# Kernel optimization log

Hardware: AMD Instinct MI355X
Metric: run time of the kernel (lower is better)

Reference implementation:

```python
import jax, jax.numpy as jnp
import numpy as np
import math

NUM_SECTORS = 8
HIDDEN = 128
FEAT = 64
MAX_DIST = 10.0


def gru_last(x, Wih, Whh, bih, bhh):
    # PyTorch GRU (gate order r,z,n); x: (B,T,D) -> last hidden (B,H)
    B = x.shape[0]
    H = Whh.shape[1]
    xp = jnp.einsum('btd,gd->btg', x, Wih) + bih  # (B,T,3H)

    def step(h, xpt):
        hp = h @ Whh.T + bhh
        xr, xz, xn = jnp.split(xpt, 3, -1)
        hr, hz, hn = jnp.split(hp, 3, -1)
        r = jax.nn.sigmoid(xr + hr)
        z = jax.nn.sigmoid(xz + hz)
        n = jnp.tanh(xn + r * hn)
        h_new = (1.0 - z) * n + z * h
        return h_new, None

    h0 = jnp.zeros((B, H), x.dtype)
    hT, _ = jax.lax.scan(step, h0, jnp.swapaxes(xp, 0, 1))
    return hT


def setup_inputs() -> dict:
    key = jax.random.key(0)
    ks = iter(jax.random.split(key, 32))
    B, N, T = 2048, 64, 8
    H, Hn = HIDDEN, HIDDEN // 2
    s = 0.05

    def p(shape):
        return jax.random.normal(next(ks), shape, jnp.float32) * s

    inp = {
        'target_trajectory': jax.random.normal(next(ks), (B, T, 2), jnp.float32),
        'neighbor_trajectories': jax.random.normal(next(ks), (B, N, T, 2), jnp.float32),
        'relative_angles': jax.random.uniform(next(ks), (B, N), jnp.float32) * (2.0 * math.pi),
        'neighbor_mask': (jax.random.uniform(next(ks), (B, N)) > 0.2).astype(jnp.float32),
        # target GRU (H=128)
        'Wih_t': p((3 * H, 2)), 'Whh_t': p((3 * H, H)), 'bih_t': p((3 * H,)), 'bhh_t': p((3 * H,)),
        # neighbor GRU (H=64)
        'Wih_n': p((3 * Hn, 2)), 'Whh_n': p((3 * Hn, Hn)), 'bih_n': p((3 * Hn,)), 'bhh_n': p((3 * Hn,)),
        # sector encoder: 68 -> 128 -> 128
        'W1': p((H, 4 + Hn)), 'b1': p((H,)), 'W2': p((H, H)), 'b2': p((H,)),
        # fusion: 1152 -> 256 -> 128 -> 64
        'Wf1': p((2 * H, H + NUM_SECTORS * H)), 'bf1': p((2 * H,)),
        'Wf2': p((H, 2 * H)), 'bf2': p((H,)),
        'Wf3': p((FEAT, H)), 'bf3': p((FEAT,)),
        'ln_g': jnp.ones((FEAT,), jnp.float32), 'ln_b': jnp.zeros((FEAT,), jnp.float32),
    }
    return inp


def reference(target_trajectory, neighbor_trajectories, relative_angles, neighbor_mask,
              Wih_t, Whh_t, bih_t, bhh_t, Wih_n, Whh_n, bih_n, bhh_n,
              W1, b1, W2, b2, Wf1, bf1, Wf2, bf2, Wf3, bf3, ln_g, ln_b):
    B, N, T, D = neighbor_trajectories.shape
    S = NUM_SECTORS

    # trajectory encoders
    target_feature = gru_last(target_trajectory, Wih_t, Whh_t, bih_t, bhh_t)  # (B,128)
    nf = gru_last(neighbor_trajectories.reshape(B * N, T, D), Wih_n, Whh_n, bih_n, bhh_n)
    nf = nf.reshape(B, N, -1)  # (B,N,64)

    # geometry
    target_pos = target_trajectory[:, -1, :]                      # (B,2)
    npos = neighbor_trajectories[:, :, -1, :]                     # (B,N,2)
    dist = jnp.linalg.norm(npos - target_pos[:, None, :], axis=-1)  # (B,N)
    vel = neighbor_trajectories[:, :, -1, :] - neighbor_trajectories[:, :, -2, :]  # (B,N,2)

    # sector assignment (vectorized segment reduce over sectors)
    sector_size = 2.0 * math.pi / S
    sid = jnp.clip((relative_angles / sector_size).astype(jnp.int32), 0, S - 1)  # (B,N)
    valid = neighbor_mask > 0
    memb = ((sid[..., None] == jnp.arange(S)) & valid[..., None]).astype(dist.dtype)  # (B,N,S)

    count = memb.sum(1)                        # (B,S)
    nonempty = count > 0
    safe = jnp.maximum(count, 1.0)
    avg_d = jnp.where(nonempty, (dist[..., None] * memb).sum(1) / safe, 0.0)  # (B,S)
    avg_v = jnp.where(nonempty[..., None], jnp.einsum('bns,bnc->bsc', memb, vel) / safe[..., None], 0.0)

    w = jnp.exp(-dist / MAX_DIST)              # (B,N)
    wm = w[..., None] * memb                   # (B,N,S)
    wsum = wm.sum(1) + 1e-8                    # (B,S)
    wfeat = jnp.einsum('bns,bnh->bsh', wm, nf) / wsum[..., None]  # (B,S,64)

    sector_feats = jnp.concatenate([count[..., None], avg_d[..., None], avg_v, wfeat], axis=-1)  # (B,S,68)

    # sector encoder MLP (dropout off / eval)
    h = jax.nn.relu(sector_feats @ W1.T + b1)
    h = jax.nn.relu(h @ W2.T + b2)             # (B,S,128)
    enc = h.reshape(B, S * HIDDEN)

    combined = jnp.concatenate([target_feature, enc], axis=-1)  # (B,1152)
    f = jax.nn.relu(combined @ Wf1.T + bf1)
    f = jax.nn.relu(f @ Wf2.T + bf2)
    f = jax.nn.relu(f @ Wf3.T + bf3)           # (B,64)

    mu = f.mean(-1, keepdims=True)
    var = ((f - mu) ** 2).mean(-1, keepdims=True)
    return (f - mu) / jnp.sqrt(var + 1e-5) * ln_g + ln_b
```

## Files before the change

### kernel.cpp

```cpp
#include <hip/hip_runtime.h>

typedef __attribute__((ext_vector_type(8))) short short8;
typedef __attribute__((ext_vector_type(4))) float f32x4;

#define SGC (-1.44269504088896341f)
#define THC ( 2.88539008177792681f)

__device__ __forceinline__ unsigned short f2bf(float f){
  unsigned u = __float_as_uint(f);
  return (unsigned short)((u + 0x7fffu + ((u >> 16) & 1u)) >> 16);
}
__device__ __forceinline__ float bf2f(unsigned short b){
  return __uint_as_float(((unsigned)b) << 16);
}
__device__ __forceinline__ unsigned f2bf_cvt(float f){
  unsigned r;
  asm("v_cvt_pk_bf16_f32 %0, %1, %1" : "=v"(r) : "v"(f));
  return r;
}

__global__ __launch_bounds__(256) void k_prep(
    const float* __restrict__ Whh_t, const float* __restrict__ W1,
    const float* __restrict__ W2,    const float* __restrict__ Wf1,
    const float* __restrict__ Wf2,   const float* __restrict__ Wf3,
    const float* __restrict__ Whh_n,
    unsigned short* __restrict__ wgt)
{
  int i = blockIdx.x * 256 + threadIdx.x;
  if (i < 49152){
    int g = i >> 7;
    float s = (g < 256) ? SGC : THC;
    wgt[i] = f2bf(Whh_t[i] * s); return;
  }
  i -= 49152;
  if (i < 12288){ int r = i / 96, c = i % 96;
    wgt[49152 + i] = (c < 68) ? f2bf(W1[r*68 + c]) : (unsigned short)0; return; }
  i -= 12288;
  if (i < 16384){ wgt[61440 + i] = f2bf(W2[i]); return; }
  i -= 16384;
  if (i < 294912){ wgt[77824 + i] = f2bf(Wf1[i]); return; }
  i -= 294912;
  if (i < 32768){ wgt[372736 + i] = f2bf(Wf2[i]); return; }
  i -= 32768;
  if (i < 8192){ wgt[405504 + i] = f2bf(Wf3[i]); return; }
  i -= 8192;
  if (i < 12288){
    int g = i >> 6;
    float s = (g < 128) ? SGC : THC;
    wgt[413696 + i] = f2bf(Whh_n[i] * s); return;
  }
}

__global__ __launch_bounds__(512, 4) void k_gru_n(
    const float* __restrict__ ttraj, const float* __restrict__ ntraj,
    const float* __restrict__ rang,  const float* __restrict__ nmask,
    const float* __restrict__ Wih_n,
    const float* __restrict__ bih_n, const float* __restrict__ bhh_n,
    const unsigned short* __restrict__ wgt,
    unsigned short* __restrict__ sf)
{
  __shared__ char smem[54272];
  const int tid = threadIdx.x;
  const int bi = tid >> 8, lt = tid & 255;
  const int w = lt >> 6, u = (lt >> 4) & 3, c = lt & 15;
  const int b = blockIdx.x * 2 + bi;
  const unsigned short* whhN_b = wgt + 413696;

  unsigned short* whh  = (unsigned short*)smem;
  char* pb = smem + 27648 + bi * 13312;
  unsigned short* hall = (unsigned short*)pb;
  unsigned short* hb   = hall + w * 1152;
  float* xst  = (float*)(pb + 9216);

  for (int i = tid; i < 1536; i += 512){
    int r = i >> 3, cg = (i & 7) * 8;
    *(short8*)&whh[r*72 + cg] = *(const short8*)&whhN_b[r*64 + cg];
  }
  {
    float4 v = ((const float4*)(ntraj + (size_t)b * 1024))[lt];
    int row = lt >> 2, p4 = (lt & 3) * 4;
    xst[(p4+0)*64 + row] = v.x;
    xst[(p4+1)*64 + row] = v.y;
    xst[(p4+2)*64 + row] = v.z;
    xst[(p4+3)*64 + row] = v.w;
  }
  __syncthreads();

  float wr0[4],wr1[4],br_[4],wz0[4],wz1[4],bz_[4],wn0[4],wn1[4],bi_[4],bh_[4];
#pragma unroll
  for (int gt = 0; gt < 4; ++gt){
    int g = gt*16 + c;
    wr0[gt]=Wih_n[g*2]*SGC;  wr1[gt]=Wih_n[g*2+1]*SGC;  br_[gt]=(bih_n[g]+bhh_n[g])*SGC;
    int gz = 64+g;  wz0[gt]=Wih_n[gz*2]*SGC; wz1[gt]=Wih_n[gz*2+1]*SGC; bz_[gt]=(bih_n[gz]+bhh_n[gz])*SGC;
    int gn = 128+g; wn0[gt]=Wih_n[gn*2]*THC; wn1[gt]=Wih_n[gn*2+1]*THC; bi_[gt]=bih_n[gn]*THC; bh_[gt]=bhh_n[gn]*THC;
  }
  float hcur[4][4];
#pragma unroll
  for (int gt=0; gt<4; ++gt)
#pragma unroll
    for (int q=0; q<4; ++q) hcur[gt][q] = 0.0f;

  float xq0[4], xq1[4];
  auto gates = [&](int gt, const f32x4& aR, const f32x4& aZ, const f32x4& aN){
#pragma unroll
    for (int q = 0; q < 4; ++q){
      float x0 = xq0[q], x1 = xq1[q];
      float rp = __builtin_fmaf(wr0[gt], x0, __builtin_fmaf(wr1[gt], x1, aR[q] + br_[gt]));
      float zp = __builtin_fmaf(wz0[gt], x0, __builtin_fmaf(wz1[gt], x1, aZ[q] + bz_[gt]));
      float r = __builtin_amdgcn_rcpf(1.0f + __builtin_amdgcn_exp2f(rp));
      float z = __builtin_amdgcn_rcpf(1.0f + __builtin_amdgcn_exp2f(zp));
      float hnv = aN[q] + bh_[gt];
      float pn = __builtin_fmaf(wn0[gt], x0, __builtin_fmaf(wn1[gt], x1, __builtin_fmaf(r, hnv, bi_[gt])));
      float E = __builtin_amdgcn_exp2f(pn);
      float n = __builtin_fmaf(-2.0f, __builtin_amdgcn_rcpf(E + 1.0f), 1.0f);
      float hnew = __builtin_fmaf(z, hcur[gt][q] - n, n);
      hcur[gt][q] = hnew;
      hb[(u*4+q)*72 + gt*16 + c] = (unsigned short)f2bf_cvt(hnew);
    }
  };

  for (int st = 0; st < 8; ++st){
#pragma unroll
    for (int q=0; q<4; ++q){
      int sq = w*16 + u*4 + q;
      xq0[q] = xst[st*128 + sq];
      xq1[q] = xst[st*128 + 64 + sq];
    }
    if (st > 0){
      short8 a0 = *(short8*)&hb[c*72 + u*8];
      short8 a1 = *(short8*)&hb[c*72 + 32 + u*8];
      f32x4 zz = {0.f,0.f,0.f,0.f};
#pragma unroll
      for (int gt = 0; gt < 4; ++gt){
        const unsigned short* pr = &whh[(gt*16+c)*72 + u*8];
        const unsigned short* pz = &whh[((4+gt)*16+c)*72 + u*8];
        const unsigned short* pq = &whh[((8+gt)*16+c)*72 + u*8];
        f32x4 aR = __builtin_amdgcn_mfma_f32_16x16x32_bf16(a0, *(const short8*)pr, zz, 0,0,0);
        aR = __builtin_amdgcn_mfma_f32_16x16x32_bf16(a1, *(const short8*)(pr+32), aR, 0,0,0);
        f32x4 aZ = __builtin_amdgcn_mfma_f32_16x16x32_bf16(a0, *(const short8*)pz, zz, 0,0,0);
        aZ = __builtin_amdgcn_mfma_f32_16x16x32_bf16(a1, *(const short8*)(pz+32), aZ, 0,0,0);
        f32x4 aN = __builtin_amdgcn_mfma_f32_16x16x32_bf16(a0, *(const short8*)pq, zz, 0,0,0);
        aN = __builtin_amdgcn_mfma_f32_16x16x32_bf16(a1, *(const short8*)(pq+32), aN, 0,0,0);
        gates(gt, aR, aZ, aN);
      }
    } else {
      f32x4 zz = {0.f,0.f,0.f,0.f};
#pragma unroll
      for (int gt = 0; gt < 4; ++gt) gates(gt, zz, zz, zz);
    }
  }
  __syncthreads();

  if (lt < 64){
    int n = lt;
    float m   = nmask[(size_t)b*64 + n];
    float ang = rang[(size_t)b*64 + n];
    float tx = ttraj[(size_t)b*16 + 14], ty = ttraj[(size_t)b*16 + 15];
    float px = xst[14*64+n], py = xst[15*64+n];
    float vx = px - xst[12*64+n], vy = py - xst[13*64+n];
    float dx = px - tx, dy = py - ty;
    float dist = __builtin_amdgcn_sqrtf(dx*dx + dy*dy);
    int sid = (int)(ang / 0.78539816339744830962f);
    sid = sid < 0 ? 0 : (sid > 7 ? 7 : sid);
    bool valid = m > 0.0f;
    float wv = valid ? __builtin_amdgcn_exp2f(dist * -0.14426950408889634f) : 0.0f;
    xst[0*64+n] = valid ? dist : 0.0f;
    xst[1*64+n] = valid ? vx   : 0.0f;
    xst[2*64+n] = valid ? vy   : 0.0f;
    xst[3*64+n] = wv;
    xst[4*64+n] = valid ? (float)sid : -1.0f;
  }
  __syncthreads();
  if (lt < 8){
    int s = lt;
    float cnt=0.f, sd=0.f, sx=0.f, sy=0.f, sw=0.f;
    for (int n=0; n<64; ++n){
      if (xst[4*64+n] == (float)s){
        cnt += 1.f; sd += xst[n]; sx += xst[64+n]; sy += xst[128+n]; sw += xst[192+n];
      }
    }
    float inv = (cnt > 0.f) ? __builtin_amdgcn_rcpf(cnt) : 0.f;
    xst[5*64+s] = cnt;
    xst[6*64+s] = sd * inv;
    xst[7*64+s] = sx * inv;
    xst[8*64+s] = sy * inv;
    xst[9*64+s] = __builtin_amdgcn_rcpf(sw + 1e-8f);
  }
  __syncthreads();
#pragma unroll
  for (int rep = 0; rep < 2; ++rep){
    int p = lt + rep*256;
    int s = p >> 6, h = p & 63;
    float fs = (float)s;
    float a = 0.f;
    for (int n = 0; n < 64; ++n){
      float wmv = (xst[4*64+n] == fs) ? xst[3*64+n] : 0.f;
      float nf  = bf2f(hall[(n>>4)*1152 + (n&15)*72 + h]);
      a += wmv * nf;
    }
    sf[((size_t)b*8 + s)*96 + 4 + h] = (unsigned short)f2bf_cvt(a * xst[9*64+s]);
  }
  if (lt < 32){
    int s = lt >> 2, cc = lt & 3;
    sf[((size_t)b*8 + s)*96 + cc] = (unsigned short)f2bf_cvt(xst[(5+cc)*64 + s]);
  }
  if (lt < 224){
    int s = lt / 28, cc = 68 + lt % 28;
    sf[((size_t)b*8 + s)*96 + cc] = 0;
  }
}

__global__ __launch_bounds__(256) void k_gru_t(
    const float* __restrict__ ttraj,
    const float* __restrict__ Wih_t, const float* __restrict__ bih_t, const float* __restrict__ bhh_t,
    const unsigned short* __restrict__ wgt,
    unsigned short* __restrict__ combined)
{
  __shared__ char smem[9728];
  const int tid = threadIdx.x, w = tid >> 6, u = (tid >> 4) & 3, c = tid & 15;
  unsigned short* hb0 = (unsigned short*)smem;
  unsigned short* hb1 = (unsigned short*)(smem + 4352);
  float* xs = (float*)(smem + 8704);

  xs[tid] = ttraj[(size_t)blockIdx.x*256 + tid];

  int ntg[6];
  ntg[0] = 2*w; ntg[1] = 2*w+1;
  ntg[2] = 8+2*w; ntg[3] = 9+2*w;
  ntg[4] = 16+2*w; ntg[5] = 17+2*w;

  short8 Bf[6][4];
#pragma unroll
  for (int lt2 = 0; lt2 < 6; ++lt2){
    const unsigned short* wp = wgt + (ntg[lt2]*16 + c)*128 + u*8;
#pragma unroll
    for (int kk = 0; kk < 4; ++kk)
      Bf[lt2][kk] = *(const short8*)(wp + kk*32);
  }

  float Wr0[2],Wr1[2],BR[2],Wz0[2],Wz1[2],BZ[2],Wn0[2],Wn1[2],BI[2],BH[2];
#pragma unroll
  for (int gt = 0; gt < 2; ++gt){
    int g = w*32 + gt*16 + c;
    Wr0[gt]=Wih_t[g*2]*SGC;        Wr1[gt]=Wih_t[g*2+1]*SGC;        BR[gt]=(bih_t[g]+bhh_t[g])*SGC;
    Wz0[gt]=Wih_t[(128+g)*2]*SGC;  Wz1[gt]=Wih_t[(128+g)*2+1]*SGC;  BZ[gt]=(bih_t[128+g]+bhh_t[128+g])*SGC;
    Wn0[gt]=Wih_t[(256+g)*2]*THC;  Wn1[gt]=Wih_t[(256+g)*2+1]*THC;  BI[gt]=bih_t[256+g]*THC; BH[gt]=bhh_t[256+g]*THC;
  }
  float hcur[2][4];
#pragma unroll
  for (int gt=0; gt<2; ++gt)
#pragma unroll
    for (int q=0; q<4; ++q) hcur[gt][q] = 0.0f;
  __syncthreads();

  for (int st = 0; st < 8; ++st){
    unsigned short* rbuf = (st & 1) ? hb0 : hb1;
    unsigned short* wbuf = (st & 1) ? hb1 : hb0;
    f32x4 acc[6];
    if (st > 0){
      short8 a0 = *(short8*)&rbuf[c*136 + u*8];
      short8 a1 = *(short8*)&rbuf[c*136 + 32 + u*8];
      short8 a2 = *(short8*)&rbuf[c*136 + 64 + u*8];
      short8 a3 = *(short8*)&rbuf[c*136 + 96 + u*8];
#pragma unroll
      for (int lt2 = 0; lt2 < 6; ++lt2){
        f32x4 t = {0.f,0.f,0.f,0.f};
        t = __builtin_amdgcn_mfma_f32_16x16x32_bf16(a0, Bf[lt2][0], t, 0,0,0);
        t = __builtin_amdgcn_mfma_f32_16x16x32_bf16(a1, Bf[lt2][1], t, 0,0,0);
        t = __builtin_amdgcn_mfma_f32_16x16x32_bf16(a2, Bf[lt2][2], t, 0,0,0);
        acc[lt2] = __builtin_amdgcn_mfma_f32_16x16x32_bf16(a3, Bf[lt2][3], t, 0,0,0);
      }
    } else {
#pragma unroll
      for (int lt2 = 0; lt2 < 6; ++lt2) acc[lt2] = (f32x4){0.f,0.f,0.f,0.f};
    }
#pragma unroll
    for (int gt = 0; gt < 2; ++gt){
#pragma unroll
      for (int q = 0; q < 4; ++q){
        int sq = u*4 + q;
        float x0 = xs[sq*16 + st*2], x1 = xs[sq*16 + st*2 + 1];
        float rp = __builtin_fmaf(Wr0[gt], x0, __builtin_fmaf(Wr1[gt], x1, acc[gt][q] + BR[gt]));
        float zp = __builtin_fmaf(Wz0[gt], x0, __builtin_fmaf(Wz1[gt], x1, acc[2+gt][q] + BZ[gt]));
        float r = __builtin_amdgcn_rcpf(1.0f + __builtin_amdgcn_exp2f(rp));
        float z = __builtin_amdgcn_rcpf(1.0f + __builtin_amdgcn_exp2f(zp));
        float hnv = acc[4+gt][q] + BH[gt];
        float pn = __builtin_fmaf(Wn0[gt], x0, __builtin_fmaf(Wn1[gt], x1, __builtin_fmaf(r, hnv, BI[gt])));
        float E = __builtin_amdgcn_exp2f(pn);
        float n = __builtin_fmaf(-2.0f, __builtin_amdgcn_rcpf(E + 1.0f), 1.0f);
        float hnew = __builtin_fmaf(z, hcur[gt][q] - n, n);
        hcur[gt][q] = hnew;
        if (st < 7){
          wbuf[sq*136 + w*32 + gt*16 + c] = (unsigned short)f2bf_cvt(hnew);
        } else {
          int row = blockIdx.x*16 + sq;
          combined[(size_t)row*1152 + w*32 + gt*16 + c] = (unsigned short)f2bf_cvt(hnew);
        }
      }
    }
    if (st < 7) __syncthreads();
  }
}

__global__ __launch_bounds__(256) void k_mlp12(
    const unsigned short* __restrict__ sf,
    const unsigned short* __restrict__ wgt,
    const float* __restrict__ b1, const float* __restrict__ b2,
    unsigned short* __restrict__ combined)
{
  __shared__ char smem[18432];
  unsigned short* hb = (unsigned short*)smem + (threadIdx.x >> 6) * 2176;
  float* b1s = (float*)(smem + 17408);
  float* b2s = b1s + 128;
  const unsigned short* w1b = wgt + 49152;
  const unsigned short* w2b = wgt + 61440;
  const int tid = threadIdx.x, w = tid >> 6, u = (tid >> 4) & 3, c = tid & 15;
  if (tid < 128){ b1s[tid] = b1[tid]; b2s[tid] = b2[tid]; }
  __syncthreads();
  const int rowb = blockIdx.x * 64 + w * 16;

  f32x4 acc[8];
#pragma unroll
  for (int nt=0; nt<8; ++nt) acc[nt] = (f32x4){0.f,0.f,0.f,0.f};
#pragma unroll
  for (int kc=0; kc<3; ++kc){
    short8 a = *(const short8*)&sf[(size_t)(rowb + c)*96 + kc*32 + u*8];
#pragma unroll
    for (int nt=0; nt<8; ++nt){
      short8 bb = *(const short8*)&w1b[(nt*16+c)*96 + kc*32 + u*8];
      acc[nt] = __builtin_amdgcn_mfma_f32_16x16x32_bf16(a, bb, acc[nt], 0,0,0);
    }
  }
#pragma unroll
  for (int nt=0; nt<8; ++nt){
    float bias = b1s[nt*16+c];
#pragma unroll
    for (int q=0; q<4; ++q){
      float v = acc[nt][q] + bias; v = v > 0.f ? v : 0.f;
      hb[(u*4+q)*136 + nt*16 + c] = (unsigned short)f2bf_cvt(v);
    }
  }
  f32x4 acc2[8];
#pragma unroll
  for (int nt=0; nt<8; ++nt) acc2[nt] = (f32x4){0.f,0.f,0.f,0.f};
#pragma unroll
  for (int kc=0; kc<4; ++kc){
    short8 a = *(short8*)&hb[c*136 + kc*32 + u*8];
#pragma unroll
    for (int nt=0; nt<8; ++nt){
      short8 bb = *(const short8*)&w2b[(nt*16+c)*128 + kc*32 + u*8];
      acc2[nt] = __builtin_amdgcn_mfma_f32_16x16x32_bf16(a, bb, acc2[nt], 0,0,0);
    }
  }
#pragma unroll
  for (int nt=0; nt<8; ++nt){
    float bias = b2s[nt*16+c];
#pragma unroll
    for (int q=0; q<4; ++q){
      float v = acc2[nt][q] + bias; v = v > 0.f ? v : 0.f;
      int r = rowb + u*4 + q;
      combined[(size_t)(r >> 3)*1152 + 128 + (r & 7)*128 + nt*16 + c] = (unsigned short)f2bf_cvt(v);
    }
  }
}

__global__ __launch_bounds__(256) void k_head(
    const unsigned short* __restrict__ combined,
    const unsigned short* __restrict__ wgt,
    const float* __restrict__ bf1, const float* __restrict__ bf2, const float* __restrict__ bf3,
    const float* __restrict__ lng, const float* __restrict__ lnb,
    float* __restrict__ out)
{
  __shared__ char smem[15104];
  const int tid = threadIdx.x, w = tid >> 6, u = (tid >> 4) & 3, c = tid & 15;
  unsigned short* f1b = (unsigned short*)smem;
  unsigned short* f2b = (unsigned short*)(smem + 8448);
  float* bf1s = (float*)(smem + 12800); float* bf2s = (float*)(smem + 13824);
  float* bf3s = (float*)(smem + 14336);
  float* lngs = (float*)(smem + 14592); float* lnbs = (float*)(smem + 14848);
  const unsigned short* wf1b = wgt + 77824;
  const unsigned short* wf2b = wgt + 372736;
  const unsigned short* wf3b = wgt + 405504;
  bf1s[tid] = bf1[tid];
  if (tid < 128) bf2s[tid] = bf2[tid];
  if (tid < 64){ bf3s[tid] = bf3[tid]; lngs[tid] = lng[tid]; lnbs[tid] = lnb[tid]; }
  __syncthreads();
  const int rowb = blockIdx.x * 16;

  f32x4 acc[4];
#pragma unroll
  for (int i=0; i<4; ++i) acc[i] = (f32x4){0.f,0.f,0.f,0.f};
#pragma unroll 4
  for (int kc=0; kc<36; ++kc){
    short8 a = *(const short8*)&combined[(size_t)(rowb + c)*1152 + kc*32 + u*8];
#pragma unroll
    for (int i=0; i<4; ++i){
      int nt = w*4 + i;
      short8 bb = *(const short8*)&wf1b[(size_t)(nt*16+c)*1152 + kc*32 + u*8];
      acc[i] = __builtin_amdgcn_mfma_f32_16x16x32_bf16(a, bb, acc[i], 0,0,0);
    }
  }
#pragma unroll
  for (int i=0; i<4; ++i){
    int nt = w*4 + i;
    float bias = bf1s[nt*16+c];
#pragma unroll
    for (int q=0; q<4; ++q){
      float v = acc[i][q] + bias; v = v > 0.f ? v : 0.f;
      f1b[(u*4+q)*264 + nt*16 + c] = (unsigned short)f2bf_cvt(v);
    }
  }
  __syncthreads();

  f32x4 acc2[2];
#pragma unroll
  for (int i=0; i<2; ++i) acc2[i] = (f32x4){0.f,0.f,0.f,0.f};
#pragma unroll
  for (int kc=0; kc<8; ++kc){
    short8 a = *(short8*)&f1b[c*264 + kc*32 + u*8];
#pragma unroll
    for (int i=0; i<2; ++i){
      int nt = w*2 + i;
      short8 bb = *(const short8*)&wf2b[(nt*16+c)*256 + kc*32 + u*8];
      acc2[i] = __builtin_amdgcn_mfma_f32_16x16x32_bf16(a, bb, acc2[i], 0,0,0);
    }
  }
#pragma unroll
  for (int i=0; i<2; ++i){
    int nt = w*2 + i;
    float bias = bf2s[nt*16+c];
#pragma unroll
    for (int q=0; q<4; ++q){
      float v = acc2[i][q] + bias; v = v > 0.f ? v : 0.f;
      f2b[(u*4+q)*136 + nt*16 + c] = (unsigned short)f2bf_cvt(v);
    }
  }
  __syncthreads();

  f32x4 acc3[4];
#pragma unroll
  for (int nt=0; nt<4; ++nt) acc3[nt] = (f32x4){0.f,0.f,0.f,0.f};
#pragma unroll
  for (int kc=0; kc<4; ++kc){
    short8 a = *(short8*)&f2b[c*136 + kc*32 + u*8];
#pragma unroll
    for (int nt=0; nt<4; ++nt){
      short8 bb = *(const short8*)&wf3b[(nt*16+c)*128 + kc*32 + u*8];
      acc3[nt] = __builtin_amdgcn_mfma_f32_16x16x32_bf16(a, bb, acc3[nt], 0,0,0);
    }
  }
  if (w == 0){
    float v[4][4];
#pragma unroll
    for (int nt=0; nt<4; ++nt){
      float bias = bf3s[nt*16+c];
#pragma unroll
      for (int q=0; q<4; ++q){
        float t = acc3[nt][q] + bias; v[nt][q] = t > 0.f ? t : 0.f;
      }
    }
#pragma unroll
    for (int q=0; q<4; ++q){
      float p = v[0][q] + v[1][q] + v[2][q] + v[3][q];
      p += __shfl_xor(p, 1); p += __shfl_xor(p, 2); p += __shfl_xor(p, 4); p += __shfl_xor(p, 8);
      float mu = p * 0.015625f;
      float d0 = v[0][q]-mu, d1 = v[1][q]-mu, d2 = v[2][q]-mu, d3 = v[3][q]-mu;
      float p2 = d0*d0 + d1*d1 + d2*d2 + d3*d3;
      p2 += __shfl_xor(p2, 1); p2 += __shfl_xor(p2, 2); p2 += __shfl_xor(p2, 4); p2 += __shfl_xor(p2, 8);
      float rstd = __builtin_amdgcn_rsqf(p2 * 0.015625f + 1e-5f);
      int row = rowb + u*4 + q;
#pragma unroll
      for (int nt=0; nt<4; ++nt){
        int col = nt*16 + c;
        out[(size_t)row*64 + col] = (v[nt][q] - mu) * rstd * lngs[col] + lnbs[col];
      }
    }
  }
}

extern "C" void kernel_launch(void* const* d_in, const int* in_sizes, int n_in,
                              void* d_out, int out_size, void* d_ws, size_t ws_size,
                              hipStream_t stream)
{
  const float* ttraj = (const float*)d_in[0];
  const float* ntraj = (const float*)d_in[1];
  const float* rang  = (const float*)d_in[2];
  const float* nmask = (const float*)d_in[3];
  const float* Wih_t = (const float*)d_in[4];
  const float* Whh_t = (const float*)d_in[5];
  const float* bih_t = (const float*)d_in[6];
  const float* bhh_t = (const float*)d_in[7];
  const float* Wih_n = (const float*)d_in[8];
  const float* Whh_n = (const float*)d_in[9];
  const float* bih_n = (const float*)d_in[10];
  const float* bhh_n = (const float*)d_in[11];
  const float* W1  = (const float*)d_in[12];
  const float* b1  = (const float*)d_in[13];
  const float* W2  = (const float*)d_in[14];
  const float* b2  = (const float*)d_in[15];
  const float* Wf1 = (const float*)d_in[16];
  const float* bf1 = (const float*)d_in[17];
  const float* Wf2 = (const float*)d_in[18];
  const float* bf2 = (const float*)d_in[19];
  const float* Wf3 = (const float*)d_in[20];
  const float* bf3 = (const float*)d_in[21];
  const float* lng = (const float*)d_in[22];
  const float* lnb = (const float*)d_in[23];

  char* ws = (char*)d_ws;
  unsigned short* combined = (unsigned short*)ws;
  unsigned short* sf       = (unsigned short*)(ws + 5242880);
  unsigned short* wgt      = (unsigned short*)(ws + 8388608);

  hipLaunchKernelGGL(k_prep, dim3(1664), dim3(256), 0, stream,
                     Whh_t, W1, W2, Wf1, Wf2, Wf3, Whh_n, wgt);
  hipLaunchKernelGGL(k_gru_n, dim3(1024), dim3(512), 0, stream,
                     ttraj, ntraj, rang, nmask, Wih_n, bih_n, bhh_n, wgt, sf);
  hipLaunchKernelGGL(k_gru_t, dim3(128), dim3(256), 0, stream,
                     ttraj, Wih_t, bih_t, bhh_t, wgt, combined);
  hipLaunchKernelGGL(k_mlp12, dim3(256), dim3(256), 0, stream, sf, wgt, b1, b2, combined);
  hipLaunchKernelGGL(k_head, dim3(128), dim3(256), 0, stream,
                     combined, wgt, bf1, bf2, bf3, lng, lnb, (float*)d_out);
}
```

Baseline: 142.9 us.

## Fold neighbor GRU input projection and biases into extra MFMA in bf16

The neighbor GRU's input projection (2 features plus a constant-1 bias column) now runs as an extra 16x16x32 bf16 MFMA per gate tile, replacing per-element scalar FMAs and the register-resident input weights. Whh is re-laid out in shared memory into an MFMA-fragment-contiguous order, and the trajectory staging buffer is reorganized so x pairs can be read as float2. This cuts VALU work and register pressure in the gate computation. In exchange it adds MFMA instructions, most lanes of which multiply zeros, and rounds the inputs, input weights and biases to bf16, which loses precision.

```diff
diff --git a/kernel.cpp b/kernel.cpp
--- a/kernel.cpp
+++ b/kernel.cpp
@@ -16,6 +16,11 @@
 __device__ __forceinline__ unsigned f2bf_cvt(float f){
   unsigned r;
   asm("v_cvt_pk_bf16_f32 %0, %1, %1" : "=v"(r) : "v"(f));
+  return r;
+}
+__device__ __forceinline__ unsigned f2bf_pk(float lo, float hi){
+  unsigned r;
+  asm("v_cvt_pk_bf16_f32 %0, %1, %2" : "=v"(r) : "v"(lo), "v"(hi));
   return r;
 }
 
@@ -66,51 +71,57 @@
   const int b = blockIdx.x * 2 + bi;
   const unsigned short* whhN_b = wgt + 413696;
 
-  unsigned short* whh  = (unsigned short*)smem;
+  unsigned short* whh2 = (unsigned short*)smem;
+  unsigned short* wx   = whh2 + 12288;
   char* pb = smem + 27648 + bi * 13312;
   unsigned short* hall = (unsigned short*)pb;
   unsigned short* hb   = hall + w * 1152;
   float* xst  = (float*)(pb + 9216);
 
   for (int i = tid; i < 1536; i += 512){
-    int r = i >> 3, cg = (i & 7) * 8;
-    *(short8*)&whh[r*72 + cg] = *(const short8*)&whhN_b[r*64 + cg];
+    int nt = i >> 7, rem = i & 127;
+    int hf = rem >> 6, uu = (rem >> 4) & 3, cc = rem & 15;
+    *(short8*)&whh2[nt*1024 + hf*512 + (uu*16+cc)*8] =
+        *(const short8*)&whhN_b[(nt*16+cc)*64 + hf*32 + uu*8];
+  }
+  if (tid < 192){
+    int t = tid >> 4, cc = tid & 15;
+    float s = (t < 8) ? SGC : THC;
+    int g = (t < 4) ? (t*16 + cc) : (t < 8) ? (64 + (t-4)*16 + cc) : (128 + (t-8)*16 + cc);
+    float bsum = (t < 8) ? (bih_n[g] + bhh_n[g]) : bih_n[g];
+    unsigned short* p = &wx[t*128 + cc*8];
+    *(short8*)p = (short8){0,0,0,0,0,0,0,0};
+    p[0] = f2bf(Wih_n[g*2]   * s);
+    p[1] = f2bf(Wih_n[g*2+1] * s);
+    p[2] = f2bf(bsum * s);
   }
   {
     float4 v = ((const float4*)(ntraj + (size_t)b * 1024))[lt];
-    int row = lt >> 2, p4 = (lt & 3) * 4;
-    xst[(p4+0)*64 + row] = v.x;
-    xst[(p4+1)*64 + row] = v.y;
-    xst[(p4+2)*64 + row] = v.z;
-    xst[(p4+3)*64 + row] = v.w;
-  }
-  __syncthreads();
-
-  float wr0[4],wr1[4],br_[4],wz0[4],wz1[4],bz_[4],wn0[4],wn1[4],bi_[4],bh_[4];
-#pragma unroll
-  for (int gt = 0; gt < 4; ++gt){
-    int g = gt*16 + c;
-    wr0[gt]=Wih_n[g*2]*SGC;  wr1[gt]=Wih_n[g*2+1]*SGC;  br_[gt]=(bih_n[g]+bhh_n[g])*SGC;
-    int gz = 64+g;  wz0[gt]=Wih_n[gz*2]*SGC; wz1[gt]=Wih_n[gz*2+1]*SGC; bz_[gt]=(bih_n[gz]+bhh_n[gz])*SGC;
-    int gn = 128+g; wn0[gt]=Wih_n[gn*2]*THC; wn1[gt]=Wih_n[gn*2+1]*THC; bi_[gt]=bih_n[gn]*THC; bh_[gt]=bhh_n[gn]*THC;
-  }
+    int seq = lt >> 2, s0 = (lt & 3) * 2;
+    xst[s0*128 + seq*2]       = v.x;
+    xst[s0*128 + seq*2 + 1]   = v.y;
+    xst[(s0+1)*128 + seq*2]   = v.z;
+    xst[(s0+1)*128 + seq*2+1] = v.w;
+  }
+  __syncthreads();
+
+  float bh_[4];
+#pragma unroll
+  for (int gt = 0; gt < 4; ++gt) bh_[gt] = bhh_n[128 + gt*16 + c] * THC;
+
   float hcur[4][4];
 #pragma unroll
   for (int gt=0; gt<4; ++gt)
 #pragma unroll
     for (int q=0; q<4; ++q) hcur[gt][q] = 0.0f;
 
-  float xq0[4], xq1[4];
-  auto gates = [&](int gt, const f32x4& aR, const f32x4& aZ, const f32x4& aN){
+  auto gates = [&](int gt, const f32x4& aR, const f32x4& aZ, const f32x4& aN, const f32x4& aX){
 #pragma unroll
     for (int q = 0; q < 4; ++q){
-      float x0 = xq0[q], x1 = xq1[q];
-      float rp = __builtin_fmaf(wr0[gt], x0, __builtin_fmaf(wr1[gt], x1, aR[q] + br_[gt]));
-      float zp = __builtin_fmaf(wz0[gt], x0, __builtin_fmaf(wz1[gt], x1, aZ[q] + bz_[gt]));
-      float r = __builtin_amdgcn_rcpf(1.0f + __builtin_amdgcn_exp2f(rp));
-      float z = __builtin_amdgcn_rcpf(1.0f + __builtin_amdgcn_exp2f(zp));
-      float hnv = aN[q] + bh_[gt];
-      float pn = __builtin_fmaf(wn0[gt], x0, __builtin_fmaf(wn1[gt], x1, __builtin_fmaf(r, hnv, bi_[gt])));
+      float r = __builtin_amdgcn_rcpf(1.0f + __builtin_amdgcn_exp2f(aR[q]));
+      float z = __builtin_amdgcn_rcpf(1.0f + __builtin_amdgcn_exp2f(aZ[q]));
+      float hn = aN[q] + bh_[gt];
+      float pn = __builtin_fmaf(r, hn, aX[q]);
       float E = __builtin_amdgcn_exp2f(pn);
       float n = __builtin_fmaf(-2.0f, __builtin_amdgcn_rcpf(E + 1.0f), 1.0f);
       float hnew = __builtin_fmaf(z, hcur[gt][q] - n, n);
@@ -119,34 +130,52 @@
     }
   };
 
+  const int lane8 = (u*16 + c) * 8;
+  const f32x4 zz = {0.f,0.f,0.f,0.f};
+
   for (int st = 0; st < 8; ++st){
-#pragma unroll
-    for (int q=0; q<4; ++q){
-      int sq = w*16 + u*4 + q;
-      xq0[q] = xst[st*128 + sq];
-      xq1[q] = xst[st*128 + 64 + sq];
-    }
+    float2 xv = *(const float2*)&xst[st*128 + (w*16+c)*2];
+    unsigned p01 = f2bf_pk(xv.x, xv.y);
+    bool u0 = (u == 0);
+    union { unsigned ui[4]; short8 s8; } a2u;
+    a2u.ui[0] = u0 ? p01 : 0u;
+    a2u.ui[1] = u0 ? 0x3F80u : 0u;
+    a2u.ui[2] = 0u; a2u.ui[3] = 0u;
+    short8 a2 = a2u.s8;
+
     if (st > 0){
       short8 a0 = *(short8*)&hb[c*72 + u*8];
       short8 a1 = *(short8*)&hb[c*72 + 32 + u*8];
-      f32x4 zz = {0.f,0.f,0.f,0.f};
 #pragma unroll
       for (int gt = 0; gt < 4; ++gt){
-        const unsigned short* pr = &whh[(gt*16+c)*72 + u*8];
-        const unsigned short* pz = &whh[((4+gt)*16+c)*72 + u*8];
-        const unsigned short* pq = &whh[((8+gt)*16+c)*72 + u*8];
+        const unsigned short* pr = whh2 + gt*1024 + lane8;
+        const unsigned short* pz = whh2 + (4+gt)*1024 + lane8;
+        const unsigned short* pq = whh2 + (8+gt)*1024 + lane8;
+        short8 bxr = *(const short8*)&wx[gt*128 + c*8];
+        short8 bxz = *(const short8*)&wx[(4+gt)*128 + c*8];
+        short8 bxn = *(const short8*)&wx[(8+gt)*128 + c*8];
         f32x4 aR = __builtin_amdgcn_mfma_f32_16x16x32_bf16(a0, *(const short8*)pr, zz, 0,0,0);
-        aR = __builtin_amdgcn_mfma_f32_16x16x32_bf16(a1, *(const short8*)(pr+32), aR, 0,0,0);
+        aR = __builtin_amdgcn_mfma_f32_16x16x32_bf16(a1, *(const short8*)(pr+512), aR, 0,0,0);
+        aR = __builtin_amdgcn_mfma_f32_16x16x32_bf16(a2, bxr, aR, 0,0,0);
         f32x4 aZ = __builtin_amdgcn_mfma_f32_16x16x32_bf16(a0, *(const short8*)pz, zz, 0,0,0);
-        aZ = __builtin_amdgcn_mfma_f32_16x16x32_bf16(a1, *(const short8*)(pz+32), aZ, 0,0,0);
+        aZ = __builtin_amdgcn_mfma_f32_16x16x32_bf16(a1, *(const short8*)(pz+512), aZ, 0,0,0);
+        aZ = __builtin_amdgcn_mfma_f32_16x16x32_bf16(a2, bxz, aZ, 0,0,0);
         f32x4 aN = __builtin_amdgcn_mfma_f32_16x16x32_bf16(a0, *(const short8*)pq, zz, 0,0,0);
-        aN = __builtin_amdgcn_mfma_f32_16x16x32_bf16(a1, *(const short8*)(pq+32), aN, 0,0,0);
-        gates(gt, aR, aZ, aN);
+        aN = __builtin_amdgcn_mfma_f32_16x16x32_bf16(a1, *(const short8*)(pq+512), aN, 0,0,0);
+        f32x4 aX = __builtin_amdgcn_mfma_f32_16x16x32_bf16(a2, bxn, zz, 0,0,0);
+        gates(gt, aR, aZ, aN, aX);
       }
     } else {
-      f32x4 zz = {0.f,0.f,0.f,0.f};
-#pragma unroll
-      for (int gt = 0; gt < 4; ++gt) gates(gt, zz, zz, zz);
+#pragma unroll
+      for (int gt = 0; gt < 4; ++gt){
+        short8 bxr = *(const short8*)&wx[gt*128 + c*8];
+        short8 bxz = *(const short8*)&wx[(4+gt)*128 + c*8];
+        short8 bxn = *(const short8*)&wx[(8+gt)*128 + c*8];
+        f32x4 aR = __builtin_amdgcn_mfma_f32_16x16x32_bf16(a2, bxr, zz, 0,0,0);
+        f32x4 aZ = __builtin_amdgcn_mfma_f32_16x16x32_bf16(a2, bxz, zz, 0,0,0);
+        f32x4 aX = __builtin_amdgcn_mfma_f32_16x16x32_bf16(a2, bxn, zz, 0,0,0);
+        gates(gt, aR, aZ, zz, aX);
+      }
     }
   }
   __syncthreads();
@@ -156,35 +185,35 @@
     float m   = nmask[(size_t)b*64 + n];
     float ang = rang[(size_t)b*64 + n];
     float tx = ttraj[(size_t)b*16 + 14], ty = ttraj[(size_t)b*16 + 15];
-    float px = xst[14*64+n], py = xst[15*64+n];
-    float vx = px - xst[12*64+n], vy = py - xst[13*64+n];
+    float px = xst[7*128 + n*2], py = xst[7*128 + n*2 + 1];
+    float vx = px - xst[6*128 + n*2], vy = py - xst[6*128 + n*2 + 1];
     float dx = px - tx, dy = py - ty;
     float dist = __builtin_amdgcn_sqrtf(dx*dx + dy*dy);
     int sid = (int)(ang / 0.78539816339744830962f);
     sid = sid < 0 ? 0 : (sid > 7 ? 7 : sid);
     bool valid = m > 0.0f;
     float wv = valid ? __builtin_amdgcn_exp2f(dist * -0.14426950408889634f) : 0.0f;
-    xst[0*64+n] = valid ? dist : 0.0f;
-    xst[1*64+n] = valid ? vx   : 0.0f;
-    xst[2*64+n] = valid ? vy   : 0.0f;
-    xst[3*64+n] = wv;
-    xst[4*64+n] = valid ? (float)sid : -1.0f;
+    xst[n]       = valid ? dist : 0.0f;
+    xst[64 + n]  = valid ? vx   : 0.0f;
+    xst[128 + n] = valid ? vy   : 0.0f;
+    xst[192 + n] = wv;
+    xst[256 + n] = valid ? (float)sid : -1.0f;
   }
   __syncthreads();
   if (lt < 8){
     int s = lt;
     float cnt=0.f, sd=0.f, sx=0.f, sy=0.f, sw=0.f;
     for (int n=0; n<64; ++n){
-      if (xst[4*64+n] == (float)s){
+      if (xst[256+n] == (float)s){
         cnt += 1.f; sd += xst[n]; sx += xst[64+n]; sy += xst[128+n]; sw += xst[192+n];
       }
     }
     float inv = (cnt > 0.f) ? __builtin_amdgcn_rcpf(cnt) : 0.f;
-    xst[5*64+s] = cnt;
-    xst[6*64+s] = sd * inv;
-    xst[7*64+s] = sx * inv;
-    xst[8*64+s] = sy * inv;
-    xst[9*64+s] = __builtin_amdgcn_rcpf(sw + 1e-8f);
+    xst[320 + s] = cnt;
+    xst[328 + s] = sd * inv;
+    xst[336 + s] = sx * inv;
+    xst[344 + s] = sy * inv;
+    xst[352 + s] = __builtin_amdgcn_rcpf(sw + 1e-8f);
   }
   __syncthreads();
 #pragma unroll
@@ -194,15 +223,15 @@
     float fs = (float)s;
     float a = 0.f;
     for (int n = 0; n < 64; ++n){
-      float wmv = (xst[4*64+n] == fs) ? xst[3*64+n] : 0.f;
+      float wmv = (xst[256+n] == fs) ? xst[192+n] : 0.f;
       float nf  = bf2f(hall[(n>>4)*1152 + (n&15)*72 + h]);
       a += wmv * nf;
     }
-    sf[((size_t)b*8 + s)*96 + 4 + h] = (unsigned short)f2bf_cvt(a * xst[9*64+s]);
+    sf[((size_t)b*8 + s)*96 + 4 + h] = (unsigned short)f2bf_cvt(a * xst[352+s]);
   }
   if (lt < 32){
     int s = lt >> 2, cc = lt & 3;
-    sf[((size_t)b*8 + s)*96 + cc] = (unsigned short)f2bf_cvt(xst[(5+cc)*64 + s]);
+    sf[((size_t)b*8 + s)*96 + cc] = (unsigned short)f2bf_cvt(xst[320 + cc*8 + s]);
   }
   if (lt < 224){
     int s = lt / 28, cc = 68 + lt % 28;
```

Measured after the change: 135.2 us. -5.4%, faster.
